# Performance work log

Measured on AMD Instinct MI355X. Metric: run time of the kernel, lower is better.

## Reference

```python
import jax, jax.numpy as jnp
import numpy as np

B, C_IN, T, N_VERTEX = 2, 64, 12, 2048
KS, C_OUT = 3, 64
NNZ = 98304  # Ks * n_vertex * avg_degree(16)


def setup_inputs() -> dict:
    key = jax.random.key(0)
    k0, k1, k2, k3, k4, k5 = jax.random.split(key, 6)
    x = jax.random.normal(k0, (B, C_IN, T, N_VERTEX), jnp.float32)
    # kaiming-uniform-ish init for weight [Ks, c_in, c_out]
    bound_w = float(np.sqrt(6.0 / C_IN))
    weight = jax.random.uniform(k1, (KS, C_IN, C_OUT), jnp.float32, -bound_w, bound_w)
    bound_b = float(1.0 / np.sqrt(C_OUT))
    bias = jax.random.uniform(k2, (C_OUT,), jnp.float32, -bound_b, bound_b)
    # sparse chebconv_filter in COO: shape [n_vertex, Ks*n_vertex]
    filter_rows = jax.random.randint(k3, (NNZ,), 0, N_VERTEX)
    filter_cols = jax.random.randint(k4, (NNZ,), 0, KS * N_VERTEX)
    filter_vals = jax.random.normal(k5, (NNZ,), jnp.float32) * 0.1
    return dict(x=x, weight=weight, bias=bias, filter_vals=filter_vals,
                filter_rows=filter_rows, filter_cols=filter_cols)


def reference(x, weight, bias, filter_vals, filter_rows, filter_cols):
    b, c_in, t, n = x.shape
    ks, _, c_out = weight.shape
    # dense GEMM: [B*T*n (row-major flatten of B,c_in,T,n keeping last dim c_in), c_in] @ [c_in, Ks*c_out]
    xw = x.reshape(-1, c_in) @ weight.reshape(c_in, ks * c_out)  # [B*c_in*T*n/c_in, Ks*c_out]
    xw = xw.reshape(n * ks, -1)                                  # [n*Ks, B*T*c_out]
    # spmm with COO filter [n, n*Ks]: gather columns, scale, scatter-add to rows
    gathered = filter_vals[:, None] * xw[filter_cols]            # [nnz, B*T*c_out]
    y = jax.ops.segment_sum(gathered, filter_rows, num_segments=N_VERTEX)  # [n, B*T*c_out]
    return y.reshape(-1, c_out) + bias                           # [n*B*T, c_out]
```

## Files before the change

kernel.cpp:

```cpp
#include <hip/hip_runtime.h>
#include <hip/hip_bf16.h>
#include <hip/hip_fp16.h>

#define NV      2048
#define NNZ_    98304
#define KDIM    64
#define WCOLS   192
#define BUCKET  128
#define CONVB   768

typedef __attribute__((ext_vector_type(8))) short  short8;
typedef __attribute__((ext_vector_type(8))) unsigned short ushort8;
typedef __attribute__((ext_vector_type(4))) float  float4v;

__device__ __forceinline__ unsigned short f2b(float f) {
    return __bfloat16_as_ushort(__float2bfloat16(f));
}
__device__ __forceinline__ unsigned int f2h2(float a, float b) {
    return (unsigned int)__half_as_ushort(__float2half(a)) |
           ((unsigned int)__half_as_ushort(__float2half(b)) << 16);
}
__device__ __forceinline__ float2 h2f2(unsigned int u) {
    const __half2 h = *reinterpret_cast<const __half2*>(&u);
    return __half22float2(h);
}

__global__ __launch_bounds__(256) void scatter_kernel(
    const int4* __restrict__ rows4, const int4* __restrict__ cols4,
    const float4* __restrict__ vals4, const float* __restrict__ wf,
    const float* __restrict__ xf,
    unsigned int* __restrict__ cnt, int2* __restrict__ sedge,
    unsigned short* __restrict__ wt, unsigned short* __restrict__ xh)
{
    const int bb = blockIdx.x;
    if (bb > NNZ_ / 1024) {
        const int cb = bb - (NNZ_ / 1024 + 1);
        const size_t base = ((size_t)cb * 256 + threadIdx.x) * 16;
        const float4* xin = (const float4*)(xf + base);
        float4 f[4];
#pragma unroll
        for (int u = 0; u < 4; u++) f[u] = xin[u];
        unsigned int p[8];
#pragma unroll
        for (int u = 0; u < 4; u++) {
            p[2 * u]     = f2h2(f[u].x, f[u].y);
            p[2 * u + 1] = f2h2(f[u].z, f[u].w);
        }
        uint4* xo = (uint4*)(xh + base);
        xo[0] = make_uint4(p[0], p[1], p[2], p[3]);
        xo[1] = make_uint4(p[4], p[5], p[6], p[7]);
        return;
    }
    if (bb == NNZ_ / 1024) {
        for (int i = 0; i < 48; i++) {
            const int e = threadIdx.x + 256 * i;
            const int k = e / WCOLS, n = e - k * WCOLS;
            wt[n * KDIM + k] = f2b(wf[e]);
        }
        return;
    }
    const int t = bb * 256 + threadIdx.x;
    const int4   r = rows4[t];
    const int4   c = cols4[t];
    const float4 v = vals4[t];
    unsigned int p;
    p = atomicAdd(&cnt[r.x], 1u); sedge[r.x * BUCKET + (p & (BUCKET - 1))] = make_int2(c.x * 512, __float_as_int(v.x));
    p = atomicAdd(&cnt[r.y], 1u); sedge[r.y * BUCKET + (p & (BUCKET - 1))] = make_int2(c.y * 512, __float_as_int(v.y));
    p = atomicAdd(&cnt[r.z], 1u); sedge[r.z * BUCKET + (p & (BUCKET - 1))] = make_int2(c.z * 512, __float_as_int(v.z));
    p = atomicAdd(&cnt[r.w], 1u); sedge[r.w * BUCKET + (p & (BUCKET - 1))] = make_int2(c.w * 512, __float_as_int(v.w));
}

__global__ __launch_bounds__(256) void fused_sg_kernel(
    const unsigned short* __restrict__ xh,
    const unsigned int* __restrict__ cnt,
    const unsigned int* __restrict__ probe,
    const int2* __restrict__ sedge,
    const unsigned short* __restrict__ wt,
    const float* __restrict__ bias, float* __restrict__ out)
{
    __shared__ unsigned short Wt[WCOLS * 72];
    __shared__ unsigned short Zs[16 * 72];
    __shared__ int2 se_lds[4][64];
    const int tid  = threadIdx.x;
    const int bid  = blockIdx.x;
    const int g    = bid & 7;
    const int v0   = (bid >> 3) * 16;
    const int w    = tid >> 6;
    const int lane = tid & 63;
    const int grp  = lane >> 4;
    const int l    = lane & 15;
    const int off  = g * KDIM + l * 4;

    const unsigned int P = probe[0];

    ushort8 wreg[6];
#pragma unroll
    for (int u = 0; u < 6; u++)
        wreg[u] = *(const ushort8*)(wt + (tid + 256 * u) * 8);

#pragma unroll 1
    for (int t = 0; t < 4; t++) {
        const int row = v0 + w * 4 + t;
        unsigned int n = cnt[row] - P;
        if (n > BUCKET) n = BUCKET;
        const int2* se = sedge + row * BUCKET;

        float a0 = 0.f, a1 = 0.f, a2 = 0.f, a3 = 0.f;
        for (unsigned int base = 0; base < n; base += 64) {
            const int m = (int)((n - base < 64) ? (n - base) : 64);
            const int li = (int)((P + base + (unsigned)((lane < m) ? lane : (m - 1))) & (BUCKET - 1));
            se_lds[w][lane] = se[li];

            int i = 0;
            for (; i + 32 <= m; i += 32) {
                int2 e[8];
#pragma unroll
                for (int u = 0; u < 8; u++) e[u] = se_lds[w][i + u * 4 + grp];
                uint2 xb[8];
#pragma unroll
                for (int u = 0; u < 8; u++) xb[u] = *(const uint2*)(xh + e[u].x + off);
#pragma unroll
                for (int u = 0; u < 8; u++) {
                    const float v = __int_as_float(e[u].y);
                    const float2 x01 = h2f2(xb[u].x), x23 = h2f2(xb[u].y);
                    a0 += v * x01.x; a1 += v * x01.y;
                    a2 += v * x23.x; a3 += v * x23.y;
                }
            }
            for (; i + 16 <= m; i += 16) {
                int2 e[4];
#pragma unroll
                for (int u = 0; u < 4; u++) e[u] = se_lds[w][i + u * 4 + grp];
                uint2 xb[4];
#pragma unroll
                for (int u = 0; u < 4; u++) xb[u] = *(const uint2*)(xh + e[u].x + off);
#pragma unroll
                for (int u = 0; u < 4; u++) {
                    const float v = __int_as_float(e[u].y);
                    const float2 x01 = h2f2(xb[u].x), x23 = h2f2(xb[u].y);
                    a0 += v * x01.x; a1 += v * x01.y;
                    a2 += v * x23.x; a3 += v * x23.y;
                }
            }
            for (; i < m; i += 4) {
                const int j  = (i + grp < m) ? (i + grp) : (m - 1);
                const int2 e = se_lds[w][j];
                const float v = (i + grp < m) ? __int_as_float(e.y) : 0.f;
                const uint2 xb = *(const uint2*)(xh + e.x + off);
                const float2 x01 = h2f2(xb.x), x23 = h2f2(xb.y);
                a0 += v * x01.x; a1 += v * x01.y;
                a2 += v * x23.x; a3 += v * x23.y;
            }
        }
        a0 += __shfl_xor(a0, 16); a1 += __shfl_xor(a1, 16);
        a2 += __shfl_xor(a2, 16); a3 += __shfl_xor(a3, 16);
        a0 += __shfl_xor(a0, 32); a1 += __shfl_xor(a1, 32);
        a2 += __shfl_xor(a2, 32); a3 += __shfl_xor(a3, 32);
        if (grp == 0) {
            uint2 o;
            o.x = (unsigned)f2b(a0) | ((unsigned)f2b(a1) << 16);
            o.y = (unsigned)f2b(a2) | ((unsigned)f2b(a3) << 16);
            *(uint2*)&Zs[(w * 4 + t) * 72 + l * 4] = o;
        }
    }

#pragma unroll
    for (int u = 0; u < 6; u++) {
        const int ch = tid + 256 * u;
        *(ushort8*)&Wt[(ch >> 3) * 72 + (ch & 7) * 8] = wreg[u];
    }
    __syncthreads();

    const int q = lane >> 4;
    const int c = lane & 15;

    const short8 a0 = *(const short8*)&Zs[c * 72 + q * 8];
    const short8 a1 = *(const short8*)&Zs[c * 72 + 32 + q * 8];

    float4v acc[3];
#pragma unroll
    for (int j = 0; j < 3; j++) {
        const int nt = w * 3 + j;
        const short8 b0 = *(const short8*)&Wt[(nt * 16 + c) * 72 + q * 8];
        const short8 b1 = *(const short8*)&Wt[(nt * 16 + c) * 72 + 32 + q * 8];
        float4v d = {0.f, 0.f, 0.f, 0.f};
        d = __builtin_amdgcn_mfma_f32_16x16x32_bf16(a0, b0, d, 0, 0, 0);
        d = __builtin_amdgcn_mfma_f32_16x16x32_bf16(a1, b1, d, 0, 0, 0);
        acc[j] = d;
    }

#pragma unroll
    for (int j = 0; j < 3; j++) {
        const int col = (w * 3 + j) * 16 + c;
        const float bb = bias[col & 63];
#pragma unroll
        for (int r = 0; r < 4; r++) {
            const int v = v0 + q * 4 + r;
            out[(size_t)(v * 8 + g) * WCOLS + col] = acc[j][r] + bb;
        }
    }
}

extern "C" void kernel_launch(void* const* d_in, const int* in_sizes, int n_in,
                              void* d_out, int out_size, void* d_ws, size_t ws_size,
                              hipStream_t stream) {
    const float* x    = (const float*)d_in[0];
    const float* wgt  = (const float*)d_in[1];
    const float* bias = (const float*)d_in[2];
    const float* fval = (const float*)d_in[3];
    const int* frow   = (const int*)d_in[4];
    const int* fcol   = (const int*)d_in[5];

    unsigned int* cnt = (unsigned int*)d_ws;
    unsigned int* probe = cnt + 2048;
    int2* sedge = (int2*)(cnt + 2112);
    unsigned short* wt = (unsigned short*)(sedge + NV * BUCKET);
    unsigned short* xh = wt + 12288;

    scatter_kernel<<<NNZ_ / 1024 + 1 + CONVB, 256, 0, stream>>>(
        (const int4*)frow, (const int4*)fcol, (const float4*)fval, wgt, x,
        cnt, sedge, wt, xh);
    fused_sg_kernel<<<1024, 256, 0, stream>>>(
        xh, cnt, probe, sedge, wt, bias, (float*)d_out);
}
```

Before: 105.0 us.

## Merge scatter and SpMM-GEMM kernels into one launch with a grid barrier

Folds the preprocessing work (x to fp16 conversion, COO edge bucketing with atomics, weight transpose to bf16) into the start of the fused gather/MFMA kernel. A software grid-wide barrier on an atomic counter separates the two phases, which removes the second kernel launch and the gap between launches. Each block now does a small slice of preprocessing, so scatter work is spread over more blocks with fewer active threads each. This relies on all 1024 blocks being co-resident (launch bounds of 4 blocks per CU) and on the counter base P persisting across calls; a spin barrier risks deadlock or stalls if residency is not guaranteed.

New measurement: 221.1 us. 2.1x slower.

```diff
diff --git a/kernel.cpp b/kernel.cpp
--- a/kernel.cpp
+++ b/kernel.cpp
@@ -7,7 +7,7 @@
 #define KDIM    64
 #define WCOLS   192
 #define BUCKET  128
-#define CONVB   768
+#define GRID_B  1024
 
 typedef __attribute__((ext_vector_type(8))) short  short8;
 typedef __attribute__((ext_vector_type(8))) unsigned short ushort8;
@@ -25,58 +25,14 @@
     return __half22float2(h);
 }
 
-__global__ __launch_bounds__(256) void scatter_kernel(
+__global__ __launch_bounds__(256, 4) void mono_kernel(
     const int4* __restrict__ rows4, const int4* __restrict__ cols4,
     const float4* __restrict__ vals4, const float* __restrict__ wf,
-    const float* __restrict__ xf,
-    unsigned int* __restrict__ cnt, int2* __restrict__ sedge,
-    unsigned short* __restrict__ wt, unsigned short* __restrict__ xh)
-{
-    const int bb = blockIdx.x;
-    if (bb > NNZ_ / 1024) {
-        const int cb = bb - (NNZ_ / 1024 + 1);
-        const size_t base = ((size_t)cb * 256 + threadIdx.x) * 16;
-        const float4* xin = (const float4*)(xf + base);
-        float4 f[4];
-#pragma unroll
-        for (int u = 0; u < 4; u++) f[u] = xin[u];
-        unsigned int p[8];
-#pragma unroll
-        for (int u = 0; u < 4; u++) {
-            p[2 * u]     = f2h2(f[u].x, f[u].y);
-            p[2 * u + 1] = f2h2(f[u].z, f[u].w);
-        }
-        uint4* xo = (uint4*)(xh + base);
-        xo[0] = make_uint4(p[0], p[1], p[2], p[3]);
-        xo[1] = make_uint4(p[4], p[5], p[6], p[7]);
-        return;
-    }
-    if (bb == NNZ_ / 1024) {
-        for (int i = 0; i < 48; i++) {
-            const int e = threadIdx.x + 256 * i;
-            const int k = e / WCOLS, n = e - k * WCOLS;
-            wt[n * KDIM + k] = f2b(wf[e]);
-        }
-        return;
-    }
-    const int t = bb * 256 + threadIdx.x;
-    const int4   r = rows4[t];
-    const int4   c = cols4[t];
-    const float4 v = vals4[t];
-    unsigned int p;
-    p = atomicAdd(&cnt[r.x], 1u); sedge[r.x * BUCKET + (p & (BUCKET - 1))] = make_int2(c.x * 512, __float_as_int(v.x));
-    p = atomicAdd(&cnt[r.y], 1u); sedge[r.y * BUCKET + (p & (BUCKET - 1))] = make_int2(c.y * 512, __float_as_int(v.y));
-    p = atomicAdd(&cnt[r.z], 1u); sedge[r.z * BUCKET + (p & (BUCKET - 1))] = make_int2(c.z * 512, __float_as_int(v.z));
-    p = atomicAdd(&cnt[r.w], 1u); sedge[r.w * BUCKET + (p & (BUCKET - 1))] = make_int2(c.w * 512, __float_as_int(v.w));
-}
-
-__global__ __launch_bounds__(256) void fused_sg_kernel(
-    const unsigned short* __restrict__ xh,
-    const unsigned int* __restrict__ cnt,
+    const float* __restrict__ xf, const float* __restrict__ bias,
+    unsigned int* __restrict__ cnt, unsigned int* __restrict__ bar,
     const unsigned int* __restrict__ probe,
-    const int2* __restrict__ sedge,
-    const unsigned short* __restrict__ wt,
-    const float* __restrict__ bias, float* __restrict__ out)
+    int2* __restrict__ sedge, unsigned short* __restrict__ wt,
+    unsigned short* __restrict__ xh, float* __restrict__ out)
 {
     __shared__ unsigned short Wt[WCOLS * 72];
     __shared__ unsigned short Zs[16 * 72];
@@ -92,6 +48,50 @@
     const int off  = g * KDIM + l * 4;
 
     const unsigned int P = probe[0];
+
+    {
+        const float4* xin = (const float4*)xf;
+        uint2* xo = (uint2*)xh;
+        const int b0 = bid * 768;
+#pragma unroll
+        for (int u = 0; u < 3; u++) {
+            const int idx = b0 + u * 256 + tid;
+            const float4 f = xin[idx];
+            uint2 o;
+            o.x = f2h2(f.x, f.y);
+            o.y = f2h2(f.z, f.w);
+            xo[idx] = o;
+        }
+    }
+    if (tid < 24) {
+        const int t = bid * 24 + tid;
+        const int4   r = rows4[t];
+        const int4   c = cols4[t];
+        const float4 v = vals4[t];
+        unsigned int p;
+        p = atomicAdd(&cnt[r.x], 1u); sedge[r.x * BUCKET + (p & (BUCKET - 1))] = make_int2(c.x * 512, __float_as_int(v.x));
+        p = atomicAdd(&cnt[r.y], 1u); sedge[r.y * BUCKET + (p & (BUCKET - 1))] = make_int2(c.y * 512, __float_as_int(v.y));
+        p = atomicAdd(&cnt[r.z], 1u); sedge[r.z * BUCKET + (p & (BUCKET - 1))] = make_int2(c.z * 512, __float_as_int(v.z));
+        p = atomicAdd(&cnt[r.w], 1u); sedge[r.w * BUCKET + (p & (BUCKET - 1))] = make_int2(c.w * 512, __float_as_int(v.w));
+    }
+    if (tid < 12) {
+        const int e = bid * 12 + tid;
+        const int k = e / WCOLS, n2 = e - k * WCOLS;
+        wt[n2 * KDIM + k] = f2b(wf[e]);
+    }
+
+    __syncthreads();
+    if (tid == 0) {
+        __threadfence();
+        atomicAdd(bar, 1u);
+        const unsigned int target = P + (unsigned int)GRID_B;
+        while (__hip_atomic_load(bar, __ATOMIC_ACQUIRE,
+                                 __HIP_MEMORY_SCOPE_AGENT) != target) {
+            __builtin_amdgcn_s_sleep(8);
+        }
+        __threadfence();
+    }
+    __syncthreads();
 
     ushort8 wreg[6];
 #pragma unroll
@@ -212,14 +212,13 @@
     const int* fcol   = (const int*)d_in[5];
 
     unsigned int* cnt = (unsigned int*)d_ws;
-    unsigned int* probe = cnt + 2048;
+    unsigned int* bar = cnt + 2048;
+    unsigned int* probe = cnt + 2052;
     int2* sedge = (int2*)(cnt + 2112);
     unsigned short* wt = (unsigned short*)(sedge + NV * BUCKET);
     unsigned short* xh = wt + 12288;
 
-    scatter_kernel<<<NNZ_ / 1024 + 1 + CONVB, 256, 0, stream>>>(
+    mono_kernel<<<GRID_B, 256, 0, stream>>>(
         (const int4*)frow, (const int4*)fcol, (const float4*)fval, wgt, x,
-        cnt, sedge, wt, xh);
-    fused_sg_kernel<<<1024, 256, 0, stream>>>(
-        xh, cnt, probe, sedge, wt, bias, (float*)d_out);
-}
+        bias, cnt, bar, probe, sedge, wt, xh, (float*)d_out);
+}
```
